# Kernel tuning notes

Hardware: AMD Instinct MI355X
Metric: run time of the kernel (lower is better)

Reference implementation:

```python
import jax, jax.numpy as jnp
import numpy as np

N_LAYERS = 8
D_MODEL = 64
D_STATE = 32
D_CONV = 4
D_INNER = 128          # expand * d_model
HEADDIM = 64
NHEADS = D_INNER // HEADDIM      # 2
CONV_DIM = D_INNER + 2 * D_STATE # 192 (x, B, C)
D_IN_PROJ = 2 * D_INNER + 2 * D_STATE + NHEADS  # 322
EPS = 1e-5


def setup_inputs() -> dict:
    key = jax.random.key(0)
    ks = jax.random.split(key, 8)
    x = jax.random.normal(ks[0], (16, 4096, D_MODEL), dtype=jnp.float32)
    Win = jax.random.normal(ks[1], (N_LAYERS, D_MODEL, D_IN_PROJ), dtype=jnp.float32) * 0.05
    conv_w = jax.random.normal(ks[2], (N_LAYERS, CONV_DIM, D_CONV), dtype=jnp.float32) * 0.2
    conv_b = jnp.zeros((N_LAYERS, CONV_DIM), dtype=jnp.float32)
    dt_bias = jax.random.uniform(ks[3], (N_LAYERS, NHEADS), minval=-4.0, maxval=-1.0)
    A_log = jnp.log(jax.random.uniform(ks[4], (N_LAYERS, NHEADS), minval=1.0, maxval=16.0))
    Dp = jnp.ones((N_LAYERS, NHEADS), dtype=jnp.float32)
    norm_w = jnp.ones((N_LAYERS, D_INNER), dtype=jnp.float32)
    Wout = jax.random.normal(ks[5], (N_LAYERS, D_INNER, D_MODEL), dtype=jnp.float32) * 0.05
    return {"x": x, "Win": Win, "conv_w": conv_w, "conv_b": conv_b,
            "dt_bias": dt_bias, "A_log": A_log, "Dp": Dp,
            "norm_w": norm_w, "Wout": Wout}


def _mamba2_layer(u, Win, conv_w, conv_b, dt_bias, A_log, Dp, norm_w, Wout):
    b, l, _ = u.shape
    zxbcdt = u @ Win                                   # (b,l,322)
    z = zxbcdt[..., :D_INNER]                          # gate (b,l,128)
    xBC = zxbcdt[..., D_INNER:D_INNER + CONV_DIM]      # (b,l,192)
    dt = jax.nn.softplus(zxbcdt[..., D_INNER + CONV_DIM:] + dt_bias)  # (b,l,H)

    # causal depthwise conv over time, then SiLU
    xc = jnp.pad(xBC.transpose(0, 2, 1), ((0, 0), (0, 0), (D_CONV - 1, 0)))
    xc = jax.lax.conv_general_dilated(
        xc, conv_w[:, None, :], (1,), 'VALID',
        feature_group_count=CONV_DIM,
        dimension_numbers=('NCH', 'OIH', 'NCH'))
    xBC = jax.nn.silu((xc + conv_b[None, :, None]).transpose(0, 2, 1))  # (b,l,192)

    xs = xBC[..., :D_INNER].reshape(b, l, NHEADS, HEADDIM)   # (b,l,h,p)
    B = xBC[..., D_INNER:D_INNER + D_STATE]                  # (b,l,n)
    C = xBC[..., D_INNER + D_STATE:]                         # (b,l,n)

    A = -jnp.exp(A_log)                                      # (h,) negative
    dA = jnp.exp(dt * A)                                     # (b,l,h)

    # sequential selective scan over time; state (b,h,p,n)
    def step(hst, inp):
        dA_t, dt_t, x_t, B_t, C_t = inp
        hst = hst * dA_t[:, :, None, None] + \
              (dt_t[:, :, None] * x_t)[..., None] * B_t[:, None, None, :]
        y_t = jnp.einsum('bhpn,bn->bhp', hst, C_t)
        return hst, y_t

    h0 = jnp.zeros((b, NHEADS, HEADDIM, D_STATE), dtype=u.dtype)
    seq = (jnp.moveaxis(dA, 1, 0), jnp.moveaxis(dt, 1, 0),
           jnp.moveaxis(xs, 1, 0), jnp.moveaxis(B, 1, 0), jnp.moveaxis(C, 1, 0))
    _, ys = jax.lax.scan(step, h0, seq)                      # (l,b,h,p)
    y = jnp.moveaxis(ys, 0, 1) + Dp[None, None, :, None] * xs  # (b,l,h,p)
    y = y.reshape(b, l, D_INNER)

    # gated RMSNorm (norm_before_gate=False): normalize after gating
    y = y * jax.nn.silu(z)
    y = y * jax.lax.rsqrt(jnp.mean(y * y, axis=-1, keepdims=True) + EPS) * norm_w
    return y @ Wout                                          # (b,l,d_model)


def reference(x, Win, conv_w, conv_b, dt_bias, A_log, Dp, norm_w, Wout):
    h = x
    for i in range(N_LAYERS - 1):
        h = _mamba2_layer(h, Win[i], conv_w[i], conv_b[i], dt_bias[i],
                          A_log[i], Dp[i], norm_w[i], Wout[i])
    h = jax.lax.stop_gradient(h)  # layers[:-1] run under torch.no_grad()
    i = N_LAYERS - 1
    return _mamba2_layer(h, Win[i], conv_w[i], conv_b[i], dt_bias[i],
                         A_log[i], Dp[i], norm_w[i], Wout[i])
```

## Files before the change

kernel.cpp:

```cpp
#include <hip/hip_runtime.h>
#include <math.h>

#define BATCH   16
#define SEQ     4096
#define DMODEL  64
#define DINNER  128
#define DSTATE  32
#define NHEADS  2
#define HEADDIM 64
#define CONVDIM 192
#define PROJ    322
#define QC      64
#define NCHUNK  (SEQ/QC)
#define BL      (BATCH*SEQ)
#define NPAD    336

typedef __attribute__((ext_vector_type(8))) short short8;
typedef __attribute__((ext_vector_type(4))) float f32x4;
typedef __attribute__((ext_vector_type(4))) unsigned short ushort4v;

__device__ inline unsigned short f2b(float f){
  union { float f; unsigned u; } v; v.f = f;
  unsigned r = v.u + 0x7FFF + ((v.u >> 16) & 1);
  return (unsigned short)(r >> 16);
}
__device__ inline float b2f(unsigned short s){
  union { unsigned u; float f; } v; v.u = ((unsigned)s) << 16; return v.f;
}
__device__ inline void split2(float x, unsigned short& h, unsigned short& l){
  unsigned short hh = f2b(x);
  h = hh;
  l = f2b(x - b2f(hh));
}

__device__ float g_z   [(size_t)BL*DINNER];
__device__ float g_y   [(size_t)BL*DINNER];
__device__ unsigned short g_C[(size_t)BL*DSTATE];
__device__ float g_cum [BATCH*NHEADS*SEQ];
__device__ float g_ctot[BATCH*NHEADS*NCHUNK];
__device__ float g_S   [BATCH*NHEADS*NCHUNK*DSTATE*HEADDIM];
__device__ float g_H   [BATCH*NHEADS*NCHUNK*DSTATE*HEADDIM];
__device__ float g_ping0[(size_t)BL*DMODEL];
__device__ float g_ping1[(size_t)BL*DMODEL];
__device__ unsigned short g_WinTh [8*NPAD*DMODEL];
__device__ unsigned short g_WinTl [8*NPAD*DMODEL];
__device__ unsigned short g_WoutTh[8*DMODEL*DINNER];
__device__ unsigned short g_WoutTl[8*DMODEL*DINNER];

__global__ __launch_bounds__(256) void k_prep(const float* __restrict__ Win,
                                              const float* __restrict__ Wout,
                                              const float* __restrict__ normw) {
  const int idx = blockIdx.x*256 + threadIdx.x;
  const int NW = 8*NPAD*DMODEL;
  if (idx < NW) {
    int layer = idx / (NPAD*DMODEL);
    int rem   = idx - layer*(NPAD*DMODEL);
    int n = rem >> 6, k = rem & 63;
    float v = (n < PROJ) ? Win[(size_t)layer*DMODEL*PROJ + k*PROJ + n] : 0.f;
    split2(v, g_WinTh[idx], g_WinTl[idx]);
  } else {
    int i2 = idx - NW;
    if (i2 < 8*DMODEL*DINNER) {
      int layer = i2 / (DMODEL*DINNER);
      int rem   = i2 - layer*(DMODEL*DINNER);
      int n = rem >> 7, k = rem & 127;
      float v = Wout[(size_t)layer*DINNER*DMODEL + k*DMODEL + n] * normw[layer*DINNER + k];
      split2(v, g_WoutTh[i2], g_WoutTl[i2]);
    }
  }
}

__global__ __launch_bounds__(256,5) void k_fusedAB(const float* __restrict__ xext, int sel,
                                                   const unsigned short* __restrict__ WinTh,
                                                   const unsigned short* __restrict__ WinTl,
                                                   const float* __restrict__ Win,
                                                   const float* __restrict__ dt_bias,
                                                   const float* __restrict__ A_log,
                                                   const float* __restrict__ conv_w,
                                                   const float* __restrict__ conv_b,
                                                   const float* __restrict__ Dp) {
  __shared__ struct {
    unsigned short Xt [64][72];
    unsigned short Bt [32][72];
    float Hl[2][5][3][66];
    union {
      struct { unsigned short Bsh[64][40]; unsigned short Csh[64][40]; } bc;
      unsigned short Gsh[64][72];
    } u;
    float dtraw[64];
  } S_;

  const float* __restrict__ X = (sel==0) ? xext : (sel==1 ? g_ping0 : g_ping1);
  const int bx = blockIdx.x; const int b = bx>>7, h = (bx>>6)&1, ch = bx&63;
  const int tid = threadIdx.x;
  const int w = tid>>6, l = tid&63, lane15 = l&15, quad = l>>4;
  const size_t row0 = (size_t)b*SEQ + (size_t)ch*QC;
  const int cbase = (b*NHEADS+h)*SEQ + ch*QC;
  const float dph = Dp[h];

  const float* xrow = &X[(row0 + 16*w + lane15)*DMODEL + quad*8];
  float4 f0 = *(const float4*)(xrow);
  float4 f1 = *(const float4*)(xrow + 4);
  float4 f2 = *(const float4*)(xrow + 32);
  float4 f3 = *(const float4*)(xrow + 36);
  short8 a0h, a0l, a1h, a1l;
  float v0[8] = {f0.x,f0.y,f0.z,f0.w,f1.x,f1.y,f1.z,f1.w};
  float v1[8] = {f2.x,f2.y,f2.z,f2.w,f3.x,f3.y,f3.z,f3.w};
  {
    unsigned short hh, ll;
#pragma unroll
    for (int j=0;j<8;j++){ split2(v0[j], hh, ll); a0h[j]=(short)hh; a0l[j]=(short)ll; }
#pragma unroll
    for (int j=0;j<8;j++){ split2(v1[j], hh, ll); a1h[j]=(short)hh; a1l[j]=(short)ll; }
  }

  {
    const float* wd = &Win[DINNER + CONVDIM + h];
    float p = 0.f;
#pragma unroll
    for (int j=0;j<8;j++) p = fmaf(v0[j], wd[(quad*8+j)*PROJ], p);
#pragma unroll
    for (int j=0;j<8;j++) p = fmaf(v1[j], wd[(32+quad*8+j)*PROJ], p);
    p += __shfl_xor(p, 16);
    p += __shfl_xor(p, 32);
    if (quad == 0) S_.dtraw[16*w + lane15] = p;
  }

  auto MFMA6 = [&](short8 A0h, short8 A1h, short8 A0l, short8 A1l, int t)->f32x4 {
    const unsigned short* bph = &WinTh[(16*t + lane15)*64 + quad*8];
    const unsigned short* bpl = &WinTl[(16*t + lane15)*64 + quad*8];
    short8 b0h = *(const short8*)bph;
    short8 b1h = *(const short8*)(bph + 32);
    short8 b0l = *(const short8*)bpl;
    short8 b1l = *(const short8*)(bpl + 32);
    f32x4 acc = {0.f,0.f,0.f,0.f};
    acc = __builtin_amdgcn_mfma_f32_16x16x32_bf16(A0h, b0h, acc, 0, 0, 0);
    acc = __builtin_amdgcn_mfma_f32_16x16x32_bf16(A1h, b1h, acc, 0, 0, 0);
    acc = __builtin_amdgcn_mfma_f32_16x16x32_bf16(A0l, b0h, acc, 0, 0, 0);
    acc = __builtin_amdgcn_mfma_f32_16x16x32_bf16(A1l, b1h, acc, 0, 0, 0);
    acc = __builtin_amdgcn_mfma_f32_16x16x32_bf16(A0h, b0l, acc, 0, 0, 0);
    acc = __builtin_amdgcn_mfma_f32_16x16x32_bf16(A1h, b1l, acc, 0, 0, 0);
    return acc;
  };

  if (ch != 0){
    const float* xh = &X[(row0 - 16 + lane15)*DMODEL + quad*8];
    float4 g0 = *(const float4*)(xh);
    float4 g1 = *(const float4*)(xh + 4);
    float4 g2 = *(const float4*)(xh + 32);
    float4 g3 = *(const float4*)(xh + 36);
    short8 e0h, e0l, e1h, e1l;
    {
      float u0[8] = {g0.x,g0.y,g0.z,g0.w,g1.x,g1.y,g1.z,g1.w};
      float u1[8] = {g2.x,g2.y,g2.z,g2.w,g3.x,g3.y,g3.z,g3.w};
      unsigned short hh, ll;
#pragma unroll
      for (int j=0;j<8;j++){ split2(u0[j], hh, ll); e0h[j]=(short)hh; e0l[j]=(short)ll; }
#pragma unroll
      for (int j=0;j<8;j++){ split2(u1[j], hh, ll); e1h[j]=(short)hh; e1l[j]=(short)ll; }
    }
    f32x4 hA = MFMA6(e0h, e1h, e0l, e1l, 8+4*h+w);
    f32x4 hB = MFMA6(e0h, e1h, e0l, e1l, 16+w);
    if (quad == 3){
#pragma unroll
      for (int r=1;r<4;r++){
        S_.Hl[0][4][r-1][w*16+lane15] = hA[r];
        S_.Hl[1][4][r-1][w*16+lane15] = hB[r];
      }
    }
  } else if (tid < 192) {
    int j = tid>>6, n = tid&63;
    S_.Hl[0][4][j][n] = 0.f;
    S_.Hl[1][4][j][n] = 0.f;
  }

  {
#pragma unroll
    for (int tt=0; tt<4; tt++){
      f32x4 az = MFMA6(a0h, a1h, a0l, a1l, 4*h+tt);
#pragma unroll
      for (int r=0;r<4;r++)
        g_z[(row0 + 16*w + quad*4 + r)*DINNER + h*64 + tt*16 + lane15] = az[r];
    }
  }

  f32x4 pa[4];
#pragma unroll
  for (int tt=0; tt<4; tt++) pa[tt] = MFMA6(a0h, a1h, a0l, a1l, 8+4*h+tt);
  if (quad == 3){
#pragma unroll
    for (int tt=0; tt<4; tt++)
#pragma unroll
      for (int r=1;r<4;r++)
        S_.Hl[0][w][r-1][tt*16+lane15] = pa[tt][r];
  }
  f32x4 pb[4];
#pragma unroll
  for (int tt=0; tt<4; tt++) pb[tt] = MFMA6(a0h, a1h, a0l, a1l, 16+tt);
  if (quad == 3){
#pragma unroll
    for (int tt=0; tt<4; tt++)
#pragma unroll
      for (int r=1;r<4;r++)
        S_.Hl[1][w][r-1][tt*16+lane15] = pb[tt][r];
  }
  __syncthreads();

  float cum, dtv, ewl;
  {
    float dr = S_.dtraw[l];
    float xv = dr + dt_bias[h];
    dtv = (xv > 20.f) ? xv : log1pf(expf(xv));
    float A = -expf(A_log[h]);
    cum = dtv * A;
#pragma unroll
    for (int off=1; off<64; off<<=1){
      float v = __shfl_up(cum, off);
      if (l >= off) cum += v;
    }
    if (w == 0){
      g_cum[cbase+l] = cum;
      if (l == 63) g_ctot[(b*NHEADS+h)*NCHUNK + ch] = cum;
    }
    float cl = __shfl(cum, 63);
    ewl = expf(cl - cum) * dtv;
  }

  const int t0 = 16*w + quad*4;

  float sv[4][4];
#pragma unroll
  for (int tt=0; tt<4; tt++){
    const int n = tt*16 + lane15;
    const int gch = h*64 + n;
    const float w0 = conv_w[gch*4+0], w1 = conv_w[gch*4+1], w2 = conv_w[gch*4+2], w3 = conv_w[gch*4+3];
    const float bb = conv_b[gch];
    float o0 = pa[tt][0], o1 = pa[tt][1], o2 = pa[tt][2], o3 = pa[tt][3];
    float p1 = __shfl_up(o3, 16), p2 = __shfl_up(o2, 16), p3 = __shfl_up(o1, 16);
    if (quad == 0){
      const int slot = (w==0) ? 4 : (w-1);
      p1 = S_.Hl[0][slot][2][n];
      p2 = S_.Hl[0][slot][1][n];
      p3 = S_.Hl[0][slot][0][n];
    }
    float c0 = fmaf(w0,p3, fmaf(w1,p2, fmaf(w2,p1, fmaf(w3,o0, bb))));
    float c1 = fmaf(w0,p2, fmaf(w1,p1, fmaf(w2,o0, fmaf(w3,o1, bb))));
    float c2 = fmaf(w0,p1, fmaf(w1,o0, fmaf(w2,o1, fmaf(w3,o2, bb))));
    float c3 = fmaf(w0,o0, fmaf(w1,o1, fmaf(w2,o2, fmaf(w3,o3, bb))));
    sv[tt][0] = c0 / (1.f + expf(-c0));
    sv[tt][1] = c1 / (1.f + expf(-c1));
    sv[tt][2] = c2 / (1.f + expf(-c2));
    sv[tt][3] = c3 / (1.f + expf(-c3));
    ushort4v xq = { f2b(sv[tt][0]), f2b(sv[tt][1]), f2b(sv[tt][2]), f2b(sv[tt][3]) };
    *(ushort4v*)&S_.Xt[n][t0] = xq;
  }

  {
    float ew0 = __shfl(ewl, t0+0), ew1 = __shfl(ewl, t0+1);
    float ew2 = __shfl(ewl, t0+2), ew3 = __shfl(ewl, t0+3);
#pragma unroll
    for (int tt=0; tt<4; tt++){
      const int nf = tt*16 + lane15;
      const int gch = 128 + nf;
      const float w0 = conv_w[gch*4+0], w1 = conv_w[gch*4+1], w2 = conv_w[gch*4+2], w3 = conv_w[gch*4+3];
      const float bb = conv_b[gch];
      float o0 = pb[tt][0], o1 = pb[tt][1], o2 = pb[tt][2], o3 = pb[tt][3];
      float p1 = __shfl_up(o3, 16), p2 = __shfl_up(o2, 16), p3 = __shfl_up(o1, 16);
      if (quad == 0){
        const int slot = (w==0) ? 4 : (w-1);
        p1 = S_.Hl[1][slot][2][nf];
        p2 = S_.Hl[1][slot][1][nf];
        p3 = S_.Hl[1][slot][0][nf];
      }
      float c0 = fmaf(w0,p3, fmaf(w1,p2, fmaf(w2,p1, fmaf(w3,o0, bb))));
      float c1 = fmaf(w0,p2, fmaf(w1,p1, fmaf(w2,o0, fmaf(w3,o1, bb))));
      float c2 = fmaf(w0,p1, fmaf(w1,o0, fmaf(w2,o1, fmaf(w3,o2, bb))));
      float c3 = fmaf(w0,o0, fmaf(w1,o1, fmaf(w2,o2, fmaf(w3,o3, bb))));
      float s0 = c0 / (1.f + expf(-c0));
      float s1 = c1 / (1.f + expf(-c1));
      float s2 = c2 / (1.f + expf(-c2));
      float s3 = c3 / (1.f + expf(-c3));
      if (tt < 2){
        const int n = nf;
        S_.u.bc.Bsh[t0+0][n] = f2b(s0);
        S_.u.bc.Bsh[t0+1][n] = f2b(s1);
        S_.u.bc.Bsh[t0+2][n] = f2b(s2);
        S_.u.bc.Bsh[t0+3][n] = f2b(s3);
        ushort4v bq = { f2b(s0*ew0), f2b(s1*ew1), f2b(s2*ew2), f2b(s3*ew3) };
        *(ushort4v*)&S_.Bt[n][t0] = bq;
      } else {
        const int n = nf - 32;
        S_.u.bc.Csh[t0+0][n] = f2b(s0);
        S_.u.bc.Csh[t0+1][n] = f2b(s1);
        S_.u.bc.Csh[t0+2][n] = f2b(s2);
        S_.u.bc.Csh[t0+3][n] = f2b(s3);
        if (h == 0){
          g_C[(row0+t0+0)*DSTATE + n] = f2b(s0);
          g_C[(row0+t0+1)*DSTATE + n] = f2b(s1);
          g_C[(row0+t0+2)*DSTATE + n] = f2b(s2);
          g_C[(row0+t0+3)*DSTATE + n] = f2b(s3);
        }
      }
    }
  }
  __syncthreads();

  short8 afr = *(const short8*)&S_.u.bc.Csh[16*w + lane15][quad*8];
  f32x4 gacc[4];
#pragma unroll
  for (int tn=0;tn<4;tn++){
    short8 bfr = *(const short8*)&S_.u.bc.Bsh[16*tn + lane15][quad*8];
    f32x4 z = {0.f,0.f,0.f,0.f};
    gacc[tn] = __builtin_amdgcn_mfma_f32_16x16x32_bf16(afr, bfr, z, 0, 0, 0);
  }
  __syncthreads();
#pragma unroll
  for (int tn=0;tn<4;tn++){
    int s = 16*tn + lane15;
    float cs = __shfl(cum, s), ds = __shfl(dtv, s);
#pragma unroll
    for (int r=0;r<4;r++){
      int t = 16*w + quad*4 + r;
      float ct = __shfl(cum, t);
      float gv = 0.f;
      if (s <= t) gv = expf(ct-cs) * ds * gacc[tn][r];
      S_.u.Gsh[t][s] = f2b(gv);
    }
  }
  __syncthreads();
#pragma unroll
  for (int tn=0;tn<4;tn++){
    f32x4 acc = {0.f,0.f,0.f,0.f};
#pragma unroll
    for (int ks=0;ks<2;ks++){
      short8 a  = *(const short8*)&S_.u.Gsh[16*w  + lane15][quad*8 + 32*ks];
      short8 bf = *(const short8*)&S_.Xt  [16*tn + lane15][quad*8 + 32*ks];
      acc = __builtin_amdgcn_mfma_f32_16x16x32_bf16(a, bf, acc, 0, 0, 0);
    }
    int p = 16*tn + lane15;
#pragma unroll
    for (int r=0;r<4;r++){
      int t = 16*w + quad*4 + r;
      g_y[(row0+t)*DINNER + h*HEADDIM + p] = acc[r] + dph * sv[tn][r];
    }
  }
  const size_t sb = (size_t)((b*NHEADS+h)*NCHUNK + ch) * (DSTATE*HEADDIM);
  const int tm2 = w & 1, tnb = (w>>1)*2;
#pragma unroll
  for (int tt=0;tt<2;tt++){
    int tn2 = tnb + tt;
    f32x4 acc = {0.f,0.f,0.f,0.f};
#pragma unroll
    for (int ks=0;ks<2;ks++){
      short8 a  = *(const short8*)&S_.Bt[16*tm2 + lane15][quad*8 + 32*ks];
      short8 bf = *(const short8*)&S_.Xt[16*tn2 + lane15][quad*8 + 32*ks];
      acc = __builtin_amdgcn_mfma_f32_16x16x32_bf16(a, bf, acc, 0, 0, 0);
    }
    int p = 16*tn2 + lane15;
#pragma unroll
    for (int r=0;r<4;r++){
      int n = 16*tm2 + quad*4 + r;
      g_S[sb + n*HEADDIM + p] = acc[r];
    }
  }
}

__global__ __launch_bounds__(256) void k_chunkScan() {
  __shared__ float dAc[NCHUNK];
  const int idx = blockIdx.x*256 + threadIdx.x;
  const int np = idx & 2047;
  const int bh = idx >> 11;
  if (threadIdx.x < NCHUNK) dAc[threadIdx.x] = expf(g_ctot[bh*NCHUNK + threadIdx.x]);
  __syncthreads();
  float h = 0.f;
  const size_t base = (size_t)bh*NCHUNK*2048 + np;
#pragma unroll 1
  for (int k0=0; k0<NCHUNK; k0+=8){
    float s[8];
#pragma unroll
    for (int j=0;j<8;j++) s[j] = g_S[base + (size_t)(k0+j)*2048];
    float hs[8];
#pragma unroll
    for (int j=0;j<8;j++){
      hs[j] = h;
      h = h*dAc[k0+j] + s[j];
    }
#pragma unroll
    for (int j=0;j<8;j++) g_H[base + (size_t)(k0+j)*2048] = hs[j];
  }
}

__global__ __launch_bounds__(256,3) void k_fusedC(const unsigned short* __restrict__ WoutTh,
                                                  const unsigned short* __restrict__ WoutTl,
                                                  float* __restrict__ dout, int dsel) {
  __shared__ float Cl[QC][DSTATE+1];
  __shared__ float ec[NHEADS][QC];
  __shared__ unsigned short yAh[64][136];
  __shared__ unsigned short yAl[64][136];
  float* __restrict__ out = (dsel==0) ? g_ping0 : (dsel==1 ? g_ping1 : dout);
  const int bx = blockIdx.x; const int b = bx>>6, ch = bx&63;
  const int tid = threadIdx.x;
  const size_t row0 = (size_t)b*SEQ + (size_t)ch*QC;
  const int w = tid>>6, l = tid&63, lane15 = l&15, quad = l>>4;
#pragma unroll
  for (int j=0;j<8;j++){ int e=tid+j*256; int s=e>>5, n=e&31;
    Cl[s][n] = b2f(g_C[(row0+s)*DSTATE + n]); }
  if (tid < 128){ int h_=tid>>6, s=tid&63;
    ec[h_][s] = expf(g_cum[(b*NHEADS+h_)*SEQ + ch*QC + s]); }
  float hr[64];
  {
    const float* H0 = &g_H[(size_t)((b*NHEADS+0)*NCHUNK + ch)*2048];
    const float* H1 = &g_H[(size_t)((b*NHEADS+1)*NCHUNK + ch)*2048];
#pragma unroll
    for (int n=0;n<32;n++){ hr[n] = H0[n*64 + l]; hr[32+n] = H1[n*64 + l]; }
  }
  __syncthreads();
#pragma unroll 2
  for (int i=0;i<16;i++){
    const int r = 16*w + i;
    const size_t row = row0 + r;
    float d0 = 0.f, d1 = 0.f;
#pragma unroll
    for (int n=0;n<32;n++){
      float c = Cl[r][n];
      d0 = fmaf(c, hr[n],    d0);
      d1 = fmaf(c, hr[32+n], d1);
    }
    float yv0 = g_y[row*DINNER + l]      + ec[0][r]*d0;
    float yv1 = g_y[row*DINNER + l + 64] + ec[1][r]*d1;
    float z0 = g_z[row*DINNER + l];
    float z1 = g_z[row*DINNER + l + 64];
    yv0 *= z0 / (1.f + expf(-z0));
    yv1 *= z1 / (1.f + expf(-z1));
    float ss = yv0*yv0 + yv1*yv1;
#pragma unroll
    for (int off=32; off>=1; off>>=1) ss += __shfl_xor(ss, off);
    float sc = rsqrtf(ss*(1.f/128.f) + 1e-5f);
    split2(yv0*sc, yAh[r][l],    yAl[r][l]);
    split2(yv1*sc, yAh[r][l+64], yAl[r][l+64]);
  }
  __syncthreads();
  short8 afh[4], afl[4];
#pragma unroll
  for (int ks=0;ks<4;ks++){
    afh[ks] = *(const short8*)&yAh[16*w + lane15][quad*8 + 32*ks];
    afl[ks] = *(const short8*)&yAl[16*w + lane15][quad*8 + 32*ks];
  }
  __syncthreads();
  float (*stgF)[68] = (float(*)[68])((float*)&yAh[0][0] + (size_t)w*16*68);
#pragma unroll
  for (int tc=0;tc<4;tc++){
    f32x4 acc = {0.f,0.f,0.f,0.f};
#pragma unroll
    for (int ks=0;ks<4;ks++){
      const unsigned short* bph = &WoutTh[(16*tc + lane15)*DINNER + quad*8 + 32*ks];
      const unsigned short* bpl = &WoutTl[(16*tc + lane15)*DINNER + quad*8 + 32*ks];
      short8 bh  = *(const short8*)bph;
      short8 blo = *(const short8*)bpl;
      acc = __builtin_amdgcn_mfma_f32_16x16x32_bf16(afh[ks], bh,  acc, 0, 0, 0);
      acc = __builtin_amdgcn_mfma_f32_16x16x32_bf16(afl[ks], bh,  acc, 0, 0, 0);
      acc = __builtin_amdgcn_mfma_f32_16x16x32_bf16(afh[ks], blo, acc, 0, 0, 0);
    }
#pragma unroll
    for (int r=0;r<4;r++)
      stgF[quad*4+r][tc*16+lane15] = acc[r];
  }
#pragma unroll
  for (int it=0; it<4; it++){
    int e = it*64 + l;
    int lr = e>>4, c4 = (e&15)<<2;
    float4 v = *(const float4*)&stgF[lr][c4];
    *(float4*)&out[(row0 + 16*w + lr)*DMODEL + c4] = v;
  }
}

extern "C" void kernel_launch(void* const* d_in, const int* in_sizes, int n_in,
                              void* d_out, int out_size, void* d_ws, size_t ws_size,
                              hipStream_t stream) {
  (void)in_sizes; (void)n_in; (void)d_ws; (void)ws_size; (void)out_size;
  const float* x       = (const float*)d_in[0];
  const float* Win     = (const float*)d_in[1];
  const float* conv_w  = (const float*)d_in[2];
  const float* conv_b  = (const float*)d_in[3];
  const float* dt_bias = (const float*)d_in[4];
  const float* A_log   = (const float*)d_in[5];
  const float* Dp      = (const float*)d_in[6];
  const float* norm_w  = (const float*)d_in[7];
  const float* Wout    = (const float*)d_in[8];

  k_prep<<<(8*(NPAD*DMODEL + DMODEL*DINNER) + 255)/256, 256, 0, stream>>>(Win, Wout, norm_w);

  unsigned short *winTh, *winTl, *woutTh, *woutTl;
  hipGetSymbolAddress((void**)&winTh,  HIP_SYMBOL(g_WinTh));
  hipGetSymbolAddress((void**)&winTl,  HIP_SYMBOL(g_WinTl));
  hipGetSymbolAddress((void**)&woutTh, HIP_SYMBOL(g_WoutTh));
  hipGetSymbolAddress((void**)&woutTl, HIP_SYMBOL(g_WoutTl));

  for (int layer = 0; layer < 8; ++layer) {
    const int insel = (layer==0) ? 0 : ((((layer-1)&1)==0) ? 1 : 2);
    const int dsel  = (layer==7) ? 2 : ((layer&1)==0 ? 0 : 1);

    k_fusedAB<<<BATCH*NHEADS*NCHUNK, 256, 0, stream>>>(x, insel,
                                        winTh + (size_t)layer*NPAD*DMODEL,
                                        winTl + (size_t)layer*NPAD*DMODEL,
                                        Win + (size_t)layer*DMODEL*PROJ,
                                        dt_bias + layer*NHEADS, A_log + layer*NHEADS,
                                        conv_w + (size_t)layer*CONVDIM*4,
                                        conv_b + (size_t)layer*CONVDIM,
                                        Dp + layer*NHEADS);
    k_chunkScan<<<(BATCH*NHEADS*DSTATE*HEADDIM)/256, 256, 0, stream>>>();
    k_fusedC<<<BATCH*NCHUNK, 256, 0, stream>>>(woutTh + (size_t)layer*DMODEL*DINNER,
                                               woutTl + (size_t)layer*DMODEL*DINNER,
                                               (float*)d_out, dsel);
  }
}
```

Baseline: 1.096 ms.

## Recompute gate z in output kernel instead of storing it to global

Removes the g_z buffer: the first kernel no longer writes the z gate projection, and the final kernel recomputes z from the layer input and Win with split-bf16 MFMA, staging it in shared memory as hi/lo bf16. This drops a large fp32 global write and read per layer in exchange for extra MFMA work, a reload of the layer input, and extra register and LDS pressure in the final kernel. Storing z as a hi/lo bf16 pair may lose a little precision compared with fp32.

```diff
diff --git a/kernel.cpp b/kernel.cpp
--- a/kernel.cpp
+++ b/kernel.cpp
@@ -33,7 +33,6 @@
   l = f2b(x - b2f(hh));
 }
 
-__device__ float g_z   [(size_t)BL*DINNER];
 __device__ float g_y   [(size_t)BL*DINNER];
 __device__ unsigned short g_C[(size_t)BL*DSTATE];
 __device__ float g_cum [BATCH*NHEADS*SEQ];
@@ -172,16 +171,6 @@
     int j = tid>>6, n = tid&63;
     S_.Hl[0][4][j][n] = 0.f;
     S_.Hl[1][4][j][n] = 0.f;
-  }
-
-  {
-#pragma unroll
-    for (int tt=0; tt<4; tt++){
-      f32x4 az = MFMA6(a0h, a1h, a0l, a1l, 4*h+tt);
-#pragma unroll
-      for (int r=0;r<4;r++)
-        g_z[(row0 + 16*w + quad*4 + r)*DINNER + h*64 + tt*16 + lane15] = az[r];
-    }
   }
 
   f32x4 pa[4];
@@ -390,18 +379,64 @@
   }
 }
 
-__global__ __launch_bounds__(256,3) void k_fusedC(const unsigned short* __restrict__ WoutTh,
+__global__ __launch_bounds__(256,3) void k_fusedC(const float* __restrict__ xext, int sel,
+                                                  const unsigned short* __restrict__ WinTh,
+                                                  const unsigned short* __restrict__ WinTl,
+                                                  const unsigned short* __restrict__ WoutTh,
                                                   const unsigned short* __restrict__ WoutTl,
                                                   float* __restrict__ dout, int dsel) {
   __shared__ float Cl[QC][DSTATE+1];
   __shared__ float ec[NHEADS][QC];
   __shared__ unsigned short yAh[64][136];
   __shared__ unsigned short yAl[64][136];
+  const float* __restrict__ X = (sel==0) ? xext : (sel==1 ? g_ping0 : g_ping1);
   float* __restrict__ out = (dsel==0) ? g_ping0 : (dsel==1 ? g_ping1 : dout);
   const int bx = blockIdx.x; const int b = bx>>6, ch = bx&63;
   const int tid = threadIdx.x;
   const size_t row0 = (size_t)b*SEQ + (size_t)ch*QC;
   const int w = tid>>6, l = tid&63, lane15 = l&15, quad = l>>4;
+
+  {
+    const float* xrow = &X[(row0 + 16*w + lane15)*DMODEL + quad*8];
+    float4 f0 = *(const float4*)(xrow);
+    float4 f1 = *(const float4*)(xrow + 4);
+    float4 f2 = *(const float4*)(xrow + 32);
+    float4 f3 = *(const float4*)(xrow + 36);
+    short8 a0h, a0l, a1h, a1l;
+    {
+      float v0[8] = {f0.x,f0.y,f0.z,f0.w,f1.x,f1.y,f1.z,f1.w};
+      float v1[8] = {f2.x,f2.y,f2.z,f2.w,f3.x,f3.y,f3.z,f3.w};
+      unsigned short hh, ll;
+#pragma unroll
+      for (int j=0;j<8;j++){ split2(v0[j], hh, ll); a0h[j]=(short)hh; a0l[j]=(short)ll; }
+#pragma unroll
+      for (int j=0;j<8;j++){ split2(v1[j], hh, ll); a1h[j]=(short)hh; a1l[j]=(short)ll; }
+    }
+#pragma unroll
+    for (int tt=0; tt<8; tt++){
+      const unsigned short* bph = &WinTh[(16*tt + lane15)*64 + quad*8];
+      const unsigned short* bpl = &WinTl[(16*tt + lane15)*64 + quad*8];
+      short8 b0h = *(const short8*)bph;
+      short8 b1h = *(const short8*)(bph + 32);
+      short8 b0l = *(const short8*)bpl;
+      short8 b1l = *(const short8*)(bpl + 32);
+      f32x4 acc = {0.f,0.f,0.f,0.f};
+      acc = __builtin_amdgcn_mfma_f32_16x16x32_bf16(a0h, b0h, acc, 0, 0, 0);
+      acc = __builtin_amdgcn_mfma_f32_16x16x32_bf16(a1h, b1h, acc, 0, 0, 0);
+      acc = __builtin_amdgcn_mfma_f32_16x16x32_bf16(a0l, b0h, acc, 0, 0, 0);
+      acc = __builtin_amdgcn_mfma_f32_16x16x32_bf16(a1l, b1h, acc, 0, 0, 0);
+      acc = __builtin_amdgcn_mfma_f32_16x16x32_bf16(a0h, b0l, acc, 0, 0, 0);
+      acc = __builtin_amdgcn_mfma_f32_16x16x32_bf16(a1h, b1l, acc, 0, 0, 0);
+#pragma unroll
+      for (int r=0;r<4;r++){
+        unsigned short hh, ll;
+        split2(acc[r], hh, ll);
+        yAh[16*w + quad*4 + r][tt*16 + lane15] = hh;
+        yAl[16*w + quad*4 + r][tt*16 + lane15] = ll;
+      }
+    }
+  }
+
 #pragma unroll
   for (int j=0;j<8;j++){ int e=tid+j*256; int s=e>>5, n=e&31;
     Cl[s][n] = b2f(g_C[(row0+s)*DSTATE + n]); }
@@ -419,6 +454,8 @@
   for (int i=0;i<16;i++){
     const int r = 16*w + i;
     const size_t row = row0 + r;
+    float z0 = b2f(yAh[r][l])    + b2f(yAl[r][l]);
+    float z1 = b2f(yAh[r][l+64]) + b2f(yAl[r][l+64]);
     float d0 = 0.f, d1 = 0.f;
 #pragma unroll
     for (int n=0;n<32;n++){
@@ -428,8 +465,6 @@
     }
     float yv0 = g_y[row*DINNER + l]      + ec[0][r]*d0;
     float yv1 = g_y[row*DINNER + l + 64] + ec[1][r]*d1;
-    float z0 = g_z[row*DINNER + l];
-    float z1 = g_z[row*DINNER + l + 64];
     yv0 *= z0 / (1.f + expf(-z0));
     yv1 *= z1 / (1.f + expf(-z1));
     float ss = yv0*yv0 + yv1*yv1;
@@ -509,7 +544,10 @@
                                         conv_b + (size_t)layer*CONVDIM,
                                         Dp + layer*NHEADS);
     k_chunkScan<<<(BATCH*NHEADS*DSTATE*HEADDIM)/256, 256, 0, stream>>>();
-    k_fusedC<<<BATCH*NCHUNK, 256, 0, stream>>>(woutTh + (size_t)layer*DMODEL*DINNER,
+    k_fusedC<<<BATCH*NCHUNK, 256, 0, stream>>>(x, insel,
+                                               winTh + (size_t)layer*NPAD*DMODEL,
+                                               winTl + (size_t)layer*NPAD*DMODEL,
+                                               woutTh + (size_t)layer*DMODEL*DINNER,
                                                woutTl + (size_t)layer*DMODEL*DINNER,
                                                (float*)d_out, dsel);
   }
```

Result: slower. 1.187 ms (+8.2%).
